# Kernel optimization log

Hardware: AMD Instinct MI355X
Metric: run time of the kernel (lower is better)

Reference implementation:

```python
import jax, jax.numpy as jnp
import numpy as np

N = 100000      # nodes
E = 1600000     # edges
NFEAT = 128
OUTF = 64
D1 = 64
D2 = 32
ALPHA = 0.2     # LeakyReLU negative slope


def setup_inputs() -> dict:
    key = jax.random.key(0)
    ks = jax.random.split(key, 12)

    def lin(k, fan_in, fan_out):
        s = 1.0 / np.sqrt(fan_in)
        kw, kb = jax.random.split(k)
        W = jax.random.uniform(kw, (fan_in, fan_out), jnp.float32, -s, s)
        b = jax.random.uniform(kb, (fan_out,), jnp.float32, -s, s)
        return W, b

    x = jax.random.normal(ks[0], (N, NFEAT), jnp.float32)
    edge_index = jax.random.randint(ks[1], (2, E), 0, N, jnp.int32)
    adj = jnp.zeros((1,), jnp.int32)  # unused by the module's forward

    W0, b0 = lin(ks[2], NFEAT, OUTF)      # self.linear
    W1, b1 = lin(ks[3], OUTF, D1)         # conv1 weight/bias
    W2, b2 = lin(ks[4], D1, D2)           # conv2 weight/bias
    W3, b3 = lin(ks[5], D2, 1)            # self.linear_2

    return {"x": x, "adj": adj, "edge_index": edge_index,
            "W0": W0, "b0": b0, "W1": W1, "b1": b1,
            "W2": W2, "b2": b2, "W3": W3, "b3": b3}


def gcn_conv(x, W, b, src, dst, n):
    """PyG GCNConv: x@W, add self-loops, sym deg-normalized scatter-add, +bias."""
    h = x @ W                                        # [n, d_out]
    loop = jnp.arange(n, dtype=src.dtype)
    s = jnp.concatenate([src, loop])                 # [E+n]
    d = jnp.concatenate([dst, loop])                 # [E+n]
    deg = jax.ops.segment_sum(jnp.ones_like(d, dtype=h.dtype), d, num_segments=n)
    dis = jnp.where(deg > 0, jax.lax.rsqrt(deg), 0.0)
    norm = dis[s] * dis[d]                           # [E+n]
    msg = h[s] * norm[:, None]                       # gather + scale
    out = jax.ops.segment_sum(msg, d, num_segments=n)
    return out + b


def reference(x, adj, edge_index, W0, b0, W1, b1, W2, b2, W3, b3):
    src, dst = edge_index[0], edge_index[1]
    # dropout layers are identity in eval mode
    h = jax.nn.leaky_relu(x @ W0 + b0, negative_slope=ALPHA)
    h = jax.nn.relu(gcn_conv(h, W1, b1, src, dst, N))
    h = jax.nn.relu(gcn_conv(h, W2, b2, src, dst, N))
    return h @ W3 + b3                               # [N, 1]
```

## Files before the change

### kernel.cpp

```cpp
#include <hip/hip_runtime.h>
#include <hip/hip_bf16.h>

#define NFEAT 128
#define ALPHA 0.2f
#define CBSH 8
#define CB   256
#define NBMAX 512
#define TILE 2048
#define BCAP 4608
#define H0STR 68

__device__ inline unsigned int packbf2(float a, float b) {
  unsigned int ua = __float_as_uint(a), ub = __float_as_uint(b);
  ua = (ua + 0x7fffu + ((ua >> 16) & 1u)) >> 16;
  ub = (ub + 0x7fffu + ((ub >> 16) & 1u)) >> 16;
  return ua | (ub << 16);
}
__device__ inline void unpackbf2(unsigned int u, float& lo, float& hi) {
  lo = __uint_as_float(u << 16);
  hi = __uint_as_float(u & 0xffff0000u);
}


__global__ __launch_bounds__(256) void k_fusedPG(
    const float* __restrict__ x, const float* __restrict__ W0, const float* __restrict__ b0,
    const float* __restrict__ W1, unsigned int* __restrict__ raw1,
    const int* __restrict__ src, const int* __restrict__ dst,
    int* __restrict__ bfill, unsigned int* __restrict__ pairs, int E, int n, int GB) {
  extern __shared__ char smem[];
  int t = threadIdx.x;
  if ((int)blockIdx.x >= GB) {
    float* h0t = (float*)smem;
    int bid = blockIdx.x - GB;
    int w = t >> 6, lane = t & 63;
    int og = __builtin_amdgcn_readfirstlane((w & 3) * 16);
    int row = bid * 64 + lane;
    bool ok = row < n;
    int rowc = ok ? row : 0;
    float acc[16];
    #pragma unroll
    for (int j = 0; j < 16; ++j) acc[j] = 0.f;
    const float4* a4 = (const float4*)(x + (size_t)rowc * NFEAT);
    const float* Wg0 = W0 + og;
    #pragma unroll 2
    for (int k4 = 0; k4 < NFEAT / 4; ++k4) {
      float4 xv = a4[k4];
      #pragma unroll
      for (int kk = 0; kk < 4; ++kk) {
        const float* wr = Wg0 + (k4 * 4 + kk) * 64;
        float xk = kk == 0 ? xv.x : kk == 1 ? xv.y : kk == 2 ? xv.z : xv.w;
        #pragma unroll
        for (int j = 0; j < 16; ++j) acc[j] += xk * wr[j];
      }
    }
    {
      float vb[16];
      #pragma unroll
      for (int j = 0; j < 16; ++j) {
        float v = acc[j] + b0[og + j];
        vb[j] = v > 0.f ? v : ALPHA * v;
      }
      float4* hw = (float4*)(h0t + lane * H0STR + og);
      hw[0] = float4{vb[0], vb[1], vb[2], vb[3]};
      hw[1] = float4{vb[4], vb[5], vb[6], vb[7]};
      hw[2] = float4{vb[8], vb[9], vb[10], vb[11]};
      hw[3] = float4{vb[12], vb[13], vb[14], vb[15]};
    }
    __syncthreads();
    float acc2[16];
    #pragma unroll
    for (int j = 0; j < 16; ++j) acc2[j] = 0.f;
    const float4* hrow = (const float4*)(h0t + lane * H0STR);
    const float* Wg1 = W1 + og;
    #pragma unroll 2
    for (int k4 = 0; k4 < 16; ++k4) {
      float4 hv = hrow[k4];
      #pragma unroll
      for (int kk = 0; kk < 4; ++kk) {
        const float* wr = Wg1 + (k4 * 4 + kk) * 64;
        float hk = kk == 0 ? hv.x : kk == 1 ? hv.y : kk == 2 ? hv.z : hv.w;
        #pragma unroll
        for (int j = 0; j < 16; ++j) acc2[j] += hk * wr[j];
      }
    }
    if (ok) {
      uint4 p0, p1;
      p0.x = packbf2(acc2[0], acc2[1]);   p0.y = packbf2(acc2[2], acc2[3]);
      p0.z = packbf2(acc2[4], acc2[5]);   p0.w = packbf2(acc2[6], acc2[7]);
      p1.x = packbf2(acc2[8], acc2[9]);   p1.y = packbf2(acc2[10], acc2[11]);
      p1.z = packbf2(acc2[12], acc2[13]); p1.w = packbf2(acc2[14], acc2[15]);
      uint4* o = (uint4*)(raw1 + (size_t)row * 32 + (og >> 1));
      o[0] = p0; o[1] = p1;
    }
    return;
  }
  unsigned long long* sp = (unsigned long long*)smem;
  int* lh = (int*)(smem + TILE * 8);
  int* lo = lh + NBMAX;
  int* gb = lo + NBMAX;
  int* lf = gb + NBMAX;
  int* wsum = lf + NBMAX;
  int tb = (int)blockIdx.x * TILE;
  int cnt = E - tb; if (cnt > TILE) cnt = TILE;
  for (int i = t; i < NBMAX; i += 256) { lh[i] = 0; lf[i] = 0; }
  __syncthreads();
  int es[TILE / 256], ed[TILE / 256];
  #pragma unroll
  for (int k = 0; k < TILE / 256; ++k) {
    int li = k * 256 + t;
    bool v = li < cnt;
    es[k] = v ? src[tb + li] : 0;
    ed[k] = v ? dst[tb + li] : -1;
    if (v) atomicAdd(&lh[ed[k] >> CBSH], 1);
  }
  __syncthreads();
  int s0 = lh[2 * t], s1 = lh[2 * t + 1];
  int ps = s0 + s1;
  wsum[t] = ps;
  __syncthreads();
  for (int o = 1; o < 256; o <<= 1) {
    int u = (t >= o) ? wsum[t - o] : 0;
    __syncthreads();
    wsum[t] += u;
    __syncthreads();
  }
  int ex = wsum[t] - ps;
  lo[2 * t] = ex;
  lo[2 * t + 1] = ex + s0;
  __syncthreads();
  for (int i = t; i < NBMAX; i += 256)
    if (lh[i] > 0) gb[i] = i * BCAP + atomicAdd(&bfill[i], lh[i]);
  __syncthreads();
  #pragma unroll
  for (int k = 0; k < TILE / 256; ++k) if (ed[k] >= 0) {
    int bb = ed[k] >> CBSH;
    int r = atomicAdd(&lf[bb], 1);
    sp[lo[bb] + r] = ((unsigned long long)(unsigned int)es[k] << 32) | (unsigned int)ed[k];
  }
  __syncthreads();
  for (int i = t; i < cnt; i += 256) {
    unsigned long long p = sp[i];
    unsigned int d = (unsigned int)p;
    unsigned int s = (unsigned int)(p >> 32);
    int bb = d >> CBSH;
    pairs[gb[bb] + (i - lo[bb])] = (s << CBSH) | (d & (CB - 1));
  }
}


__global__ __launch_bounds__(256) void k_bcsr(const unsigned int* __restrict__ pairs,
    const int* __restrict__ bcnt, int* __restrict__ rowS, int* __restrict__ rowC,
    int* __restrict__ lst, float* __restrict__ dis, int n) {
  __shared__ int deg[CB];
  __shared__ int woff[4];
  int b = blockIdx.x, t = threadIdx.x;
  int lane = t & 63, w = t >> 6;
  int beg = b * BCAP, end = beg + bcnt[b];
  deg[t] = 0;
  __syncthreads();
  for (int i = beg + t; i < end; i += 256)
    atomicAdd(&deg[pairs[i] & (CB - 1)], 1);
  __syncthreads();
  int d = deg[t];
  int v = d;
  #pragma unroll
  for (int o = 1; o < 64; o <<= 1) {
    int u = __shfl_up(v, o);
    if (lane >= o) v += u;
  }
  if (lane == 63) woff[w] = v;
  __syncthreads();
  if (t == 0) {
    int s = 0;
    #pragma unroll
    for (int k = 0; k < 4; ++k) { int x = woff[k]; woff[k] = s; s += x; }
  }
  __syncthreads();
  int pos = beg + (v - d) + woff[w];
  int node = (b << CBSH) + t;
  if (node < n) {
    rowS[node] = pos;
    rowC[node] = d;
    dis[node] = rsqrtf((float)(d + 1));
  }
  __syncthreads();
  deg[t] = pos;
  __syncthreads();
  for (int i = beg + t; i < end; i += 256) {
    unsigned int u = pairs[i];
    int p = atomicAdd(&deg[u & (CB - 1)], 1);
    lst[p] = (int)(u >> CBSH);
  }
}


__global__ __launch_bounds__(256) void k_gemm2(const float* __restrict__ A,
    const float* __restrict__ W, const float* __restrict__ dis,
    unsigned int* __restrict__ outv, int n) {
  constexpr int WPC = 2;
  constexpr int RPB = 2 * 64;
  int w = threadIdx.x >> 6, lane = threadIdx.x & 63;
  int og = __builtin_amdgcn_readfirstlane((w % WPC) * 16);
  int row = blockIdx.x * RPB + (w / WPC) * 64 + lane;
  bool ok = row < n;
  int rowc = ok ? row : 0;
  float acc[16];
  #pragma unroll
  for (int j = 0; j < 16; ++j) acc[j] = 0.f;
  const float4* a4 = (const float4*)(A + (size_t)rowc * 64);
  const float* Wg = W + og;
  #pragma unroll 4
  for (int k4 = 0; k4 < 16; ++k4) {
    float4 xv = a4[k4];
    #pragma unroll
    for (int kk = 0; kk < 4; ++kk) {
      const float* wr = Wg + (k4 * 4 + kk) * 32;
      float xk = kk == 0 ? xv.x : kk == 1 ? xv.y : kk == 2 ? xv.z : xv.w;
      #pragma unroll
      for (int j = 0; j < 16; ++j) acc[j] += xk * wr[j];
    }
  }
  if (!ok) return;
  float sc = dis[rowc];
  #pragma unroll
  for (int j = 0; j < 16; ++j) acc[j] *= sc;
  uint4 p0, p1;
  p0.x = packbf2(acc[0], acc[1]);   p0.y = packbf2(acc[2], acc[3]);
  p0.z = packbf2(acc[4], acc[5]);   p0.w = packbf2(acc[6], acc[7]);
  p1.x = packbf2(acc[8], acc[9]);   p1.y = packbf2(acc[10], acc[11]);
  p1.z = packbf2(acc[12], acc[13]); p1.w = packbf2(acc[14], acc[15]);
  uint4* o = (uint4*)(outv + (((size_t)row * 32 + og) >> 1));
  o[0] = p0; o[1] = p1;
}


__global__ __launch_bounds__(256) void k_agg1(const uint4* __restrict__ g4,
    const float* __restrict__ dis, const float* __restrict__ bias,
    const int* __restrict__ rowS, const int* __restrict__ rowC, const int* __restrict__ lst,
    float* __restrict__ h, int n) {
  int wid = (blockIdx.x * 256 + threadIdx.x) >> 6;
  if (wid >= n) return;
  int lane = threadIdx.x & 63;
  int c = lane & 7, q = lane >> 3;
  float dd = dis[wid];
  float a[8];
  #pragma unroll
  for (int j = 0; j < 8; ++j) a[j] = 0.f;
  if (q == 0) {
    uint4 u = g4[(size_t)wid * 8 + c];
    float l, hv;
    unpackbf2(u.x, l, hv); a[0] = dd * l; a[1] = dd * hv;
    unpackbf2(u.y, l, hv); a[2] = dd * l; a[3] = dd * hv;
    unpackbf2(u.z, l, hv); a[4] = dd * l; a[5] = dd * hv;
    unpackbf2(u.w, l, hv); a[6] = dd * l; a[7] = dd * hv;
  }
  int beg = rowS[wid], cnt = rowC[wid];
  for (int o = q; o < cnt; o += 32) {
    int s[4]; uint4 u[4]; float ds[4];
    #pragma unroll
    for (int k = 0; k < 4; ++k)
      s[k] = (o + 8 * k < cnt) ? lst[beg + o + 8 * k] : -1;
    #pragma unroll
    for (int k = 0; k < 4; ++k) {
      u[k] = (s[k] >= 0) ? g4[(size_t)s[k] * 8 + c] : uint4{0u, 0u, 0u, 0u};
      ds[k] = (s[k] >= 0) ? dis[s[k]] : 0.f;
    }
    #pragma unroll
    for (int k = 0; k < 4; ++k) {
      float l, hv;
      unpackbf2(u[k].x, l, hv); a[0] = fmaf(ds[k], l, a[0]); a[1] = fmaf(ds[k], hv, a[1]);
      unpackbf2(u[k].y, l, hv); a[2] = fmaf(ds[k], l, a[2]); a[3] = fmaf(ds[k], hv, a[3]);
      unpackbf2(u[k].z, l, hv); a[4] = fmaf(ds[k], l, a[4]); a[5] = fmaf(ds[k], hv, a[5]);
      unpackbf2(u[k].w, l, hv); a[6] = fmaf(ds[k], l, a[6]); a[7] = fmaf(ds[k], hv, a[7]);
    }
  }
  #pragma unroll
  for (int j = 0; j < 8; ++j) {
    a[j] += __shfl_xor(a[j], 32);
    a[j] += __shfl_xor(a[j], 16);
    a[j] += __shfl_xor(a[j], 8);
  }
  if (q == 0) {
    float vb[8];
    #pragma unroll
    for (int j = 0; j < 8; ++j) {
      float v = dd * a[j] + bias[8 * c + j];
      vb[j] = v > 0.f ? v : 0.f;
    }
    float4* hp = (float4*)(h + (size_t)wid * 64 + 8 * c);
    hp[0] = float4{vb[0], vb[1], vb[2], vb[3]};
    hp[1] = float4{vb[4], vb[5], vb[6], vb[7]};
  }
}

__global__ __launch_bounds__(256) void k_agg2(const uint4* __restrict__ g4,
    const float* __restrict__ dis, const float* __restrict__ bias,
    const float* __restrict__ W3, const float* __restrict__ b3,
    const int* __restrict__ rowS, const int* __restrict__ rowC, const int* __restrict__ lst,
    float* __restrict__ out, int n) {
  int wid = (blockIdx.x * 256 + threadIdx.x) >> 6;
  if (wid >= n) return;
  int lane = threadIdx.x & 63;
  int c = lane & 3, q = lane >> 2;
  float a[8];
  #pragma unroll
  for (int j = 0; j < 8; ++j) a[j] = 0.f;
  if (q == 0) {
    uint4 u = g4[(size_t)wid * 4 + c];
    unpackbf2(u.x, a[0], a[1]); unpackbf2(u.y, a[2], a[3]);
    unpackbf2(u.z, a[4], a[5]); unpackbf2(u.w, a[6], a[7]);
  }
  int beg = rowS[wid], cnt = rowC[wid];
  for (int o = q; o < cnt; o += 32) {
    int s[2]; uint4 u[2];
    #pragma unroll
    for (int k = 0; k < 2; ++k)
      s[k] = (o + 16 * k < cnt) ? lst[beg + o + 16 * k] : -1;
    #pragma unroll
    for (int k = 0; k < 2; ++k)
      u[k] = (s[k] >= 0) ? g4[(size_t)s[k] * 4 + c] : uint4{0u, 0u, 0u, 0u};
    #pragma unroll
    for (int k = 0; k < 2; ++k) {
      float l, hv;
      unpackbf2(u[k].x, l, hv); a[0] += l; a[1] += hv;
      unpackbf2(u[k].y, l, hv); a[2] += l; a[3] += hv;
      unpackbf2(u[k].z, l, hv); a[4] += l; a[5] += hv;
      unpackbf2(u[k].w, l, hv); a[6] += l; a[7] += hv;
    }
  }
  #pragma unroll
  for (int j = 0; j < 8; ++j) {
    a[j] += __shfl_xor(a[j], 32);
    a[j] += __shfl_xor(a[j], 16);
    a[j] += __shfl_xor(a[j], 8);
    a[j] += __shfl_xor(a[j], 4);
  }
  float d = dis[wid];
  float r = 0.f;
  #pragma unroll
  for (int j = 0; j < 8; ++j) {
    float v = d * a[j] + bias[8 * c + j];
    v = v > 0.f ? v : 0.f;
    r += v * W3[8 * c + j];
  }
  r += __shfl_xor(r, 2);
  r += __shfl_xor(r, 1);
  if (lane == 0) out[wid] = r + b3[0];
}


extern "C" void kernel_launch(void* const* d_in, const int* in_sizes, int n_in,
                              void* d_out, int out_size, void* d_ws, size_t ws_size,
                              hipStream_t stream) {
  (void)n_in; (void)out_size; (void)ws_size;
  const float* x  = (const float*)d_in[0];
  const int*   ei = (const int*)d_in[2];
  const float* W0 = (const float*)d_in[3];
  const float* b0 = (const float*)d_in[4];
  const float* W1 = (const float*)d_in[5];
  const float* b1 = (const float*)d_in[6];
  const float* W2 = (const float*)d_in[7];
  const float* b2 = (const float*)d_in[8];
  const float* W3 = (const float*)d_in[9];
  const float* b3 = (const float*)d_in[10];
  float* out = (float*)d_out;
  int N = in_sizes[0] / NFEAT;
  int E = in_sizes[2] / 2;
  const int* src = ei;
  const int* dst = ei + E;
  int nbuk = (N + CB - 1) / CB;

  char* ws = (char*)d_ws;
  size_t off = 0;
  auto alloc = [&](size_t bytes) -> char* {
    char* p = ws + off;
    off += (bytes + 255) & ~(size_t)255;
    return p;
  };
  int*   bfill = (int*)alloc((size_t)NBMAX * 4);
  int*   rowS  = (int*)alloc((size_t)N * 4);
  int*   rowC  = (int*)alloc((size_t)N * 4);
  float* dis   = (float*)alloc((size_t)N * 4);
  unsigned int* pairs = (unsigned int*)alloc((size_t)nbuk * BCAP * 4);
  int*   lst   = (int*)alloc((size_t)nbuk * BCAP * 4);
  float* bufA  = (float*)alloc((size_t)N * 64 * 4);
  unsigned int* bufG = (unsigned int*)alloc((size_t)N * 32 * 4);

  int GB  = (E + TILE - 1) / TILE;
  int G01 = (N + 63) / 64;
  constexpr int SMEM = TILE * 8 + NBMAX * 4 * 4 + 256 * 4;

  hipMemsetAsync(bfill, 0, (size_t)nbuk * 4, stream);
  k_fusedPG<<<GB + G01, 256, SMEM, stream>>>(x, W0, b0, W1, bufG, src, dst, bfill, pairs, E, N, GB);
  k_bcsr<<<nbuk, 256, 0, stream>>>(pairs, bfill, rowS, rowC, lst, dis, N);
  k_agg1<<<(N + 3) / 4, 256, 0, stream>>>((const uint4*)bufG, dis, b1, rowS, rowC, lst, bufA, N);
  k_gemm2<<<(N + 127) / 128, 256, 0, stream>>>(bufA, W2, dis, bufG, N);
  k_agg2<<<(N + 3) / 4, 256, 0, stream>>>((const uint4*)bufG, dis, b2, W3, b3, rowS, rowC, lst, out, N);
}
```

Baseline: 187.9 us.

## Scatter edge pairs directly using atomic rank, drop LDS staging and scan

New measurement: 184.5 us. Within noise of the previous version (-1.9%).

```diff
diff --git a/kernel.cpp b/kernel.cpp
--- a/kernel.cpp
+++ b/kernel.cpp
@@ -6,7 +6,7 @@
 #define CBSH 8
 #define CB   256
 #define NBMAX 512
-#define TILE 2048
+#define TILE 4096
 #define BCAP 4608
 #define H0STR 68
 
@@ -94,39 +94,21 @@
     }
     return;
   }
-  unsigned long long* sp = (unsigned long long*)smem;
-  int* lh = (int*)(smem + TILE * 8);
-  int* lo = lh + NBMAX;
-  int* gb = lo + NBMAX;
-  int* lf = gb + NBMAX;
-  int* wsum = lf + NBMAX;
+  int* lh = (int*)smem;
+  int* gb = lh + NBMAX;
   int tb = (int)blockIdx.x * TILE;
   int cnt = E - tb; if (cnt > TILE) cnt = TILE;
-  for (int i = t; i < NBMAX; i += 256) { lh[i] = 0; lf[i] = 0; }
-  __syncthreads();
-  int es[TILE / 256], ed[TILE / 256];
+  for (int i = t; i < NBMAX; i += 256) lh[i] = 0;
+  __syncthreads();
+  int es[TILE / 256], ed[TILE / 256], rk[TILE / 256];
   #pragma unroll
   for (int k = 0; k < TILE / 256; ++k) {
     int li = k * 256 + t;
     bool v = li < cnt;
     es[k] = v ? src[tb + li] : 0;
     ed[k] = v ? dst[tb + li] : -1;
-    if (v) atomicAdd(&lh[ed[k] >> CBSH], 1);
-  }
-  __syncthreads();
-  int s0 = lh[2 * t], s1 = lh[2 * t + 1];
-  int ps = s0 + s1;
-  wsum[t] = ps;
-  __syncthreads();
-  for (int o = 1; o < 256; o <<= 1) {
-    int u = (t >= o) ? wsum[t - o] : 0;
-    __syncthreads();
-    wsum[t] += u;
-    __syncthreads();
-  }
-  int ex = wsum[t] - ps;
-  lo[2 * t] = ex;
-  lo[2 * t + 1] = ex + s0;
+    rk[k] = v ? atomicAdd(&lh[ed[k] >> CBSH], 1) : 0;
+  }
   __syncthreads();
   for (int i = t; i < NBMAX; i += 256)
     if (lh[i] > 0) gb[i] = i * BCAP + atomicAdd(&bfill[i], lh[i]);
@@ -134,16 +116,7 @@
   #pragma unroll
   for (int k = 0; k < TILE / 256; ++k) if (ed[k] >= 0) {
     int bb = ed[k] >> CBSH;
-    int r = atomicAdd(&lf[bb], 1);
-    sp[lo[bb] + r] = ((unsigned long long)(unsigned int)es[k] << 32) | (unsigned int)ed[k];
-  }
-  __syncthreads();
-  for (int i = t; i < cnt; i += 256) {
-    unsigned long long p = sp[i];
-    unsigned int d = (unsigned int)p;
-    unsigned int s = (unsigned int)(p >> 32);
-    int bb = d >> CBSH;
-    pairs[gb[bb] + (i - lo[bb])] = (s << CBSH) | (d & (CB - 1));
+    pairs[gb[bb] + rk[k]] = ((unsigned int)es[k] << CBSH) | (unsigned int)(ed[k] & (CB - 1));
   }
 }
 
@@ -388,7 +361,7 @@
 
   int GB  = (E + TILE - 1) / TILE;
   int G01 = (N + 63) / 64;
-  constexpr int SMEM = TILE * 8 + NBMAX * 4 * 4 + 256 * 4;
+  constexpr int SMEM = 64 * H0STR * 4;
 
   hipMemsetAsync(bfill, 0, (size_t)nbuk * 4, stream);
   k_fusedPG<<<GB + G01, 256, SMEM, stream>>>(x, W0, b0, W1, bufG, src, dst, bfill, pairs, E, N, GB);
```
